# Kernel tuning notes

Hardware: AMD Instinct MI355X
Metric: run time of the kernel (lower is better)

The kernel has to match this reference:

```python
import jax, jax.numpy as jnp
import numpy as np

N, M, ND, K = 80000, 150000, 10000, 27  # active voxels, 2D painted points, downscaled voxels, 3x3x3 kernel
C3, C2, CP = 16, 64, 259                # 3D ch (stage 1), 2D conv ch, painted 2D feature ch
CM, CO = C3 + C2, 32 + 64               # mixed ch (80), downscale out ch (96)


def subm_conv(feats, nbr, W):
    """Submanifold sparse conv as gather + per-offset GEMM.
    feats: [N_in, Cin], nbr: [N_out, K] int (-1 = missing), W: [K, Cin, Cout]."""
    out = jnp.zeros((nbr.shape[0], W.shape[-1]), feats.dtype)
    for k in range(W.shape[0]):  # fixed small kernel loop (27)
        idx = nbr[:, k]
        g = jnp.where((idx >= 0)[:, None], feats[jnp.clip(idx, 0)], 0.0)
        out = out + g @ W[k]
    return out


def bn_relu(x, gamma, beta):  # folded eval-mode BN1d + ReLU
    return jax.nn.relu(x * gamma + beta)


def setup_inputs() -> dict:
    key = jax.random.key(0)
    ks = jax.random.split(key, 24)

    def w(k, shape, fan_in):
        return jax.random.normal(k, shape, jnp.float32) * (1.0 / np.sqrt(fan_in))

    inp = {
        'x3d': jax.random.normal(ks[0], (N, C3), jnp.float32),
        'f2d': jax.random.normal(ks[1], (M, CP), jnp.float32),
        'nn_idx': jax.random.randint(ks[2], (N,), -1, M, jnp.int32),     # -1 = no 2D match
        'nbr': jax.random.randint(ks[3], (N, K), -1, N, jnp.int32),      # -1 = missing neighbor
        'nbr_ds': jax.random.randint(ks[4], (ND, K), -1, N, jnp.int32),
        'W3d': w(ks[5], (K, C3, C3), K * C3),
        'g3d': jnp.ones((C3,), jnp.float32), 'b3d': jnp.zeros((C3,), jnp.float32),
        'Wg': w(ks[6], (C3, CP), C3), 'bg': jnp.zeros((CP,), jnp.float32),
        'Wc': w(ks[7], (C3, CP), C3), 'bc': jnp.zeros((CP,), jnp.float32),
        'Wp': w(ks[8], (CP, C2), CP),
        'W2d': w(ks[9], (K, C2, C2), K * C2),
        'g2d': jnp.ones((C2,), jnp.float32), 'b2d': jnp.zeros((C2,), jnp.float32),
        'Wm1': w(ks[10], (K, CM, CM), K * CM),
        'gm1': jnp.ones((CM,), jnp.float32), 'bm1': jnp.zeros((CM,), jnp.float32),
        'Wm2': w(ks[11], (K, CM, CM), K * CM),
        'gm2': jnp.ones((CM,), jnp.float32), 'bm2': jnp.zeros((CM,), jnp.float32),
        'Wa1': w(ks[12], (K, CM, CM), K * CM),
        'ga1': jnp.ones((CM,), jnp.float32), 'ba1': jnp.zeros((CM,), jnp.float32),
        'Wa2': w(ks[13], (K, CM, CM), K * CM),
        'ga2': jnp.ones((CM,), jnp.float32), 'ba2': jnp.zeros((CM,), jnp.float32),
        'Wds': w(ks[14], (K, CM, CO), K * CM),
        'gds': jnp.ones((CO,), jnp.float32), 'bds': jnp.zeros((CO,), jnp.float32),
    }
    return inp


def reference(x3d, f2d, nn_idx, nbr, nbr_ds,
              W3d, g3d, b3d, Wg, bg, Wc, bc, Wp,
              W2d, g2d, b2d,
              Wm1, gm1, bm1, Wm2, gm2, bm2,
              Wa1, ga1, ba1, Wa2, ga2, ba2,
              Wds, gds, bds):
    # irregular gather of painted 2D features to voxel sites (NN index, -1 invalid)
    f2g = jnp.where((nn_idx >= 0)[:, None], f2d[jnp.clip(nn_idx, 0)], 0.0)  # [N, 259]

    # 3D branch: SubMConv3d(C3->C3) + BN + ReLU
    y3d = bn_relu(subm_conv(x3d, nbr, W3d), g3d, b3d)                       # [N, 16]

    # per-stage gate / cross-gate (Linear + ReLU) on 3D features, applied to raw 2D feats
    gate = jax.nn.relu(y3d @ Wg + bg)                                       # [N, 259]
    cross = jax.nn.relu(y3d @ Wc + bc)                                      # [N, 259]

    # gated 2D branch: project gated painted feats to 64, SubMConv3d + BN + ReLU
    p2d = (gate * f2g) @ Wp                                                 # [N, 64]
    x2d = bn_relu(subm_conv(p2d, nbr, W2d), g2d, b2d)                       # [N, 64]
    cross2d = (cross * f2g) @ Wp                                            # [N, 64]

    # cross-modal mix + SparseBasicBlock (residual, two subm convs)
    mix = jnp.concatenate([y3d, x2d + cross2d], axis=-1)                    # [N, 80]
    h = bn_relu(subm_conv(mix, nbr, Wm1), gm1, bm1)
    h = jax.nn.relu(subm_conv(h, nbr, Wm2) * gm2 + bm2 + mix)

    # aggregation SparseBasicBlock
    a = bn_relu(subm_conv(h, nbr, Wa1), ga1, ba1)
    a = jax.nn.relu(subm_conv(a, nbr, Wa2) * ga2 + ba2 + h)

    # strided SparseConv3d downscale (gather from input sites at new out sites)
    out = bn_relu(subm_conv(a, nbr_ds, Wds), gds, bds)                      # [ND, 96]
    return out
```

## Files before the change

### kernel.cpp

```cpp
#include <hip/hip_runtime.h>

#define NPTS 80000
#define MPTS 150000
#define NDPTS 10000
#define KOFF 27
#define C3 16
#define CP 259
#define C2 64
#define CM 80
#define CO 96

typedef __attribute__((ext_vector_type(8))) short short8;
typedef __attribute__((ext_vector_type(4))) float f32x4;

__device__ inline short bf16r(float f) {
  union { float f; unsigned u; } x{f};
  unsigned r = (x.u + 0x7fffu + ((x.u >> 16) & 1u)) >> 16;
  return (short)r;
}

__global__ void wfrag_kernel(const float* __restrict__ W, short* __restrict__ WbfF,
                             int CIN, int COUT_, int KC) {
  const int NT = COUT_ / 16;
  int i = blockIdx.x * 256 + threadIdx.x;
  int total = KOFF * KC * NT * 512;
  if (i >= total) return;
  int j = i & 7, lane = (i >> 3) & 63;
  int rest = i >> 9;
  int t = rest % NT; rest /= NT;
  int q = rest % KC;
  int k = rest / KC;
  int ci = q * 32 + (lane >> 4) * 8 + j;
  int n = t * 16 + (lane & 15);
  float v = (ci < CIN) ? W[((size_t)k * CIN + ci) * COUT_ + n] : 0.f;
  WbfF[i] = bf16r(v);
}

__global__ void wpfrag_kernel(const float* __restrict__ Wp, short* __restrict__ WpF) {
  int i = blockIdx.x * 256 + threadIdx.x;
  if (i >= 9 * 4 * 64 * 8) return;
  int j = i & 7, lane = (i >> 3) & 63, t = (i >> 9) & 3, q = i >> 11;
  int k = q * 32 + (lane >> 4) * 8 + j;
  int n = t * 16 + (lane & 15);
  WpF[i] = (k < CP) ? bf16r(Wp[(size_t)k * C2 + n]) : (short)0;
}

__global__ __launch_bounds__(256) void conv3d_bnrelu_kernel(
    const float* __restrict__ x3d, const int* __restrict__ nbr,
    const float* __restrict__ W3d, const float* __restrict__ g3d,
    const float* __restrict__ b3d, float* __restrict__ y3d,
    float* __restrict__ mix, short* __restrict__ mixbf)
{
  __shared__ float wS[KOFF * C3 * C3];
  __shared__ float fS[16][C3];
  const int tid = threadIdx.x;
  const int base = blockIdx.x * 16;
  for (int e = tid; e < KOFF * C3 * C3; e += 256) wS[e] = W3d[e];
  const int r = tid >> 4, c = tid & 15;
  const int row = base + r;
  float acc = 0.f;
  for (int k = 0; k < KOFF; ++k) {
    int idx = nbr[row * KOFF + k];
    float fv = (idx >= 0) ? x3d[idx * C3 + c] : 0.f;
    __syncthreads();
    fS[r][c] = fv;
    __syncthreads();
    const float* wk = &wS[k * C3 * C3];
    #pragma unroll
    for (int ci = 0; ci < C3; ++ci)
      acc = fmaf(fS[r][ci], wk[ci * C3 + c], acc);
  }
  float v = fmaxf(fmaf(acc, g3d[c], b3d[c]), 0.f);
  y3d[row * C3 + c] = v;
  mix[row * CM + c] = v;
  mixbf[row * CM + c] = bf16r(v);
}

__global__ __launch_bounds__(256) void gate_cross_mfma_kernel(
    const float* __restrict__ y3d, const float* __restrict__ f2d,
    const int* __restrict__ nn_idx,
    const float* __restrict__ Wg, const float* __restrict__ bg,
    const float* __restrict__ Wc, const float* __restrict__ bc,
    const short* __restrict__ WpF,
    short* __restrict__ p2dbf, float* __restrict__ cross2d)
{
  constexpr int RS = 296;
  __shared__ short g1S[32 * RS];
  __shared__ short g2S[32 * RS];
  __shared__ float yS[32][C3];
  const int tid = threadIdx.x;
  const int lane = tid & 63;
  const int w = tid >> 6;
  const int lm = lane & 15;
  const int quad = lane >> 4;
  const int base = blockIdx.x * 32;

  for (int e = tid; e < 32 * 32; e += 256) {
    int r = e >> 5, cc = 256 + (e & 31);
    if (cc >= CP) {
      g1S[r * RS + cc] = 0;
      g2S[r * RS + cc] = 0;
    }
  }

  int ix[32];
  #pragma unroll
  for (int r = 0; r < 32; ++r) ix[r] = nn_idx[base + r];

  const int c = tid;
  float f[32];
  #pragma unroll
  for (int r = 0; r < 32; ++r)
    f[r] = (ix[r] >= 0) ? f2d[(size_t)ix[r] * CP + c] : 0.f;

  float ftail = 0.f;
  int tr = 0, tcc = 0;
  if (tid < 96) {
    tr = tid / 3; tcc = tid - tr * 3;
    if (ix[tr] >= 0) ftail = f2d[(size_t)ix[tr] * CP + 256 + tcc];
  }

  for (int e = tid; e < 32 * C3; e += 256)
    ((float*)yS)[e] = y3d[(size_t)base * C3 + e];

  float wg[16], wc[16];
  #pragma unroll
  for (int ci = 0; ci < 16; ++ci) {
    wg[ci] = Wg[ci * CP + c];
    wc[ci] = Wc[ci * CP + c];
  }
  const float bgv = bg[c], bcv = bc[c];

  __syncthreads();

  #pragma unroll
  for (int r = 0; r < 32; ++r) {
    float a1 = bgv, a2 = bcv;
    #pragma unroll
    for (int ci = 0; ci < 16; ++ci) {
      float yv = yS[r][ci];
      a1 = fmaf(yv, wg[ci], a1);
      a2 = fmaf(yv, wc[ci], a2);
    }
    g1S[r * RS + c] = bf16r(fmaxf(a1, 0.f) * f[r]);
    g2S[r * RS + c] = bf16r(fmaxf(a2, 0.f) * f[r]);
  }

  if (tid < 96) {
    const int c2 = 256 + tcc;
    float a1 = bg[c2], a2 = bc[c2];
    #pragma unroll
    for (int ci = 0; ci < 16; ++ci) {
      float yv = yS[tr][ci];
      a1 = fmaf(yv, Wg[ci * CP + c2], a1);
      a2 = fmaf(yv, Wc[ci * CP + c2], a2);
    }
    g1S[tr * RS + c2] = bf16r(fmaxf(a1, 0.f) * ftail);
    g2S[tr * RS + c2] = bf16r(fmaxf(a2, 0.f) * ftail);
  }
  __syncthreads();

  const int gsel = w & 1;
  const int mt = w >> 1;
  const short* gS = gsel ? g2S : g1S;
  f32x4 acc[4];
  #pragma unroll
  for (int t = 0; t < 4; ++t) {
    f32x4 z = {0.f, 0.f, 0.f, 0.f};
    acc[t] = z;
  }
  #pragma unroll
  for (int q = 0; q < 9; ++q) {
    short8 af = *(const short8*)&gS[(mt * 16 + lm) * RS + q * 32 + quad * 8];
    #pragma unroll
    for (int t = 0; t < 4; ++t) {
      short8 bf = *(const short8*)&WpF[(((q * 4 + t) * 64) + lane) * 8];
      acc[t] = __builtin_amdgcn_mfma_f32_16x16x32_bf16(af, bf, acc[t], 0, 0, 0);
    }
  }
  #pragma unroll
  for (int t = 0; t < 4; ++t) {
    const int cc = t * 16 + lm;
    #pragma unroll
    for (int rg = 0; rg < 4; ++rg) {
      const int row = base + mt * 16 + quad * 4 + rg;
      float v = acc[t][rg];
      if (gsel == 0)
        p2dbf[(size_t)row * C2 + cc] = bf16r(v);
      else
        cross2d[(size_t)row * C2 + cc] = v;
    }
  }
}

template <int CIN, int COUT_, int MODE, int MT>
__global__ __launch_bounds__(64, 2) void conv_nolds_kernel(
    const short* __restrict__ finbf, const int* __restrict__ nbr, int nrows,
    const short* __restrict__ WbfF, const float* __restrict__ gamma,
    const float* __restrict__ beta, const float* __restrict__ resf,
    float* __restrict__ outf, short* __restrict__ outbf)
{
  constexpr int KC = (CIN + 31) / 32;
  constexpr int DCH = CIN / 8;
  constexpr int NT = COUT_ / 16;

  const int lane = threadIdx.x;
  const int lm = lane & 15;
  const int quad = lane >> 4;
  const int base = blockIdx.x * (MT * 16);

  int rrow[MT];
  bool rok[MT];
  #pragma unroll
  for (int i = 0; i < MT; ++i) {
    rrow[i] = base + i * 16 + lm;
    rok[i] = rrow[i] < nrows;
  }

  f32x4 acc[MT][NT];
  #pragma unroll
  for (int i = 0; i < MT; ++i)
    #pragma unroll
    for (int t = 0; t < NT; ++t) {
      f32x4 z = {0.f, 0.f, 0.f, 0.f};
      acc[i][t] = z;
    }

  const short8 zero8 = {0, 0, 0, 0, 0, 0, 0, 0};

  auto loadIdx = [&](int (&id)[MT], int k) {
    #pragma unroll
    for (int i = 0; i < MT; ++i)
      id[i] = (k < KOFF && rok[i]) ? nbr[(size_t)rrow[i] * KOFF + k] : -1;
  };

  auto loadA = [&](short8 (&pa)[MT][KC], const int (&id)[MT]) {
    #pragma unroll
    for (int i = 0; i < MT; ++i) {
      const int safe = (id[i] < 0) ? 0 : id[i];
      const bool ok = id[i] >= 0;
      const short* src = finbf + (size_t)safe * CIN;
      #pragma unroll
      for (int q = 0; q < KC; ++q) {
        const int ch = q * 4 + quad;
        short8 v = zero8;
        if (ch < DCH) v = *(const short8*)(src + ch * 8);
        pa[i][q] = ok ? v : zero8;
      }
    }
  };

  auto computeK = [&](const short8 (&pa)[MT][KC], int k) {
    const short* wb = WbfF + ((size_t)k * KC * NT) * 512 + lane * 8;
    #pragma unroll
    for (int q = 0; q < KC; ++q) {
      #pragma unroll
      for (int t = 0; t < NT; ++t) {
        short8 bfr = *(const short8*)(wb + (q * NT + t) * 512);
        #pragma unroll
        for (int i = 0; i < MT; ++i)
          acc[i][t] = __builtin_amdgcn_mfma_f32_16x16x32_bf16(pa[i][q], bfr,
                                                              acc[i][t], 0, 0, 0);
      }
    }
  };

  int ia[MT], ib[MT], ic[MT];
  short8 paA[MT][KC], paB[MT][KC], paC[MT][KC];

  loadIdx(ia, 0); loadIdx(ib, 1); loadIdx(ic, 2);
  loadA(paA, ia); loadIdx(ia, 3);
  loadA(paB, ib); loadIdx(ib, 4);

  for (int kk = 0; kk < KOFF; kk += 3) {
    loadA(paC, ic); loadIdx(ic, kk + 5);
    computeK(paA, kk);
    loadA(paA, ia); loadIdx(ia, kk + 6);
    computeK(paB, kk + 1);
    loadA(paB, ib); loadIdx(ib, kk + 7);
    computeK(paC, kk + 2);
  }

  #pragma unroll
  for (int i = 0; i < MT; ++i) {
    int rbase = base + i * 16 + quad * 4;
    #pragma unroll
    for (int t = 0; t < NT; ++t) {
      int cc = t * 16 + lm;
      float g = gamma[cc], b = beta[cc];
      #pragma unroll
      for (int rg = 0; rg < 4; ++rg) {
        int row = rbase + rg;
        if (row >= nrows) continue;
        float v = acc[i][t][rg];
        if (MODE == 0) {
          outf[(size_t)row * COUT_ + cc] = fmaxf(fmaf(v, g, b), 0.f);
        } else if (MODE == 1) {
          outbf[(size_t)row * COUT_ + cc] = bf16r(fmaxf(fmaf(v, g, b), 0.f));
        } else if (MODE == 2) {
          float o = fmaxf(fmaf(v, g, b), 0.f) + resf[(size_t)row * C2 + cc];
          outf[(size_t)row * CM + 16 + cc] = o;
          outbf[(size_t)row * CM + 16 + cc] = bf16r(o);
        } else if (MODE == 3) {
          float o = fmaxf(fmaf(v, g, b) + resf[(size_t)row * COUT_ + cc], 0.f);
          outf[(size_t)row * COUT_ + cc] = o;
          outbf[(size_t)row * COUT_ + cc] = bf16r(o);
        } else {
          float o = fmaxf(fmaf(v, g, b) + resf[(size_t)row * COUT_ + cc], 0.f);
          outbf[(size_t)row * COUT_ + cc] = bf16r(o);
        }
      }
    }
  }
}

extern "C" void kernel_launch(void* const* d_in, const int* in_sizes, int n_in,
                              void* d_out, int out_size, void* d_ws, size_t ws_size,
                              hipStream_t stream) {
  const float* x3d  = (const float*)d_in[0];
  const float* f2d  = (const float*)d_in[1];
  const int*   nn   = (const int*)d_in[2];
  const int*   nbr  = (const int*)d_in[3];
  const int*   nbds = (const int*)d_in[4];
  const float* W3d  = (const float*)d_in[5];
  const float* g3d  = (const float*)d_in[6];
  const float* b3d  = (const float*)d_in[7];
  const float* Wg   = (const float*)d_in[8];
  const float* bg   = (const float*)d_in[9];
  const float* Wc   = (const float*)d_in[10];
  const float* bc   = (const float*)d_in[11];
  const float* Wp   = (const float*)d_in[12];
  const float* W2d  = (const float*)d_in[13];
  const float* g2d  = (const float*)d_in[14];
  const float* b2d  = (const float*)d_in[15];
  const float* Wm1  = (const float*)d_in[16];
  const float* gm1  = (const float*)d_in[17];
  const float* bm1  = (const float*)d_in[18];
  const float* Wm2  = (const float*)d_in[19];
  const float* gm2  = (const float*)d_in[20];
  const float* bm2  = (const float*)d_in[21];
  const float* Wa1  = (const float*)d_in[22];
  const float* ga1  = (const float*)d_in[23];
  const float* ba1  = (const float*)d_in[24];
  const float* Wa2  = (const float*)d_in[25];
  const float* ga2  = (const float*)d_in[26];
  const float* ba2  = (const float*)d_in[27];
  const float* Wds  = (const float*)d_in[28];
  const float* gds  = (const float*)d_in[29];
  const float* bds  = (const float*)d_in[30];

  const size_t N = NPTS;
  float* ws = (float*)d_ws;
  float* y3d     = ws;
  short* p2dbf   = (short*)(ws + N * 16);
  float* cross2d = ws + N * 48;
  float* mix     = ws + N * 112;
  short* mixbf   = (short*)(ws + N * 192);
  short* tmp1bf  = (short*)(ws + N * 232);
  float* hbuf    = ws + N * 272;
  short* hbufbf  = (short*)(ws + N * 352);
  short* abufbf  = (short*)ws;
  short* wtail  = (short*)(ws + N * 392);
  short* WbfF2d = wtail;
  short* WbfFm1 = WbfF2d + 110592;
  short* WbfFm2 = WbfFm1 + 207360;
  short* WbfFa1 = WbfFm2 + 207360;
  short* WbfFa2 = WbfFa1 + 207360;
  short* WbfFds = WbfFa2 + 207360;
  short* WpF    = WbfFds + 248832;

  wfrag_kernel<<<(110592 + 255) / 256, 256, 0, stream>>>(W2d, WbfF2d, 64, 64, 2);
  wfrag_kernel<<<(207360 + 255) / 256, 256, 0, stream>>>(Wm1, WbfFm1, 80, 80, 3);
  wfrag_kernel<<<(207360 + 255) / 256, 256, 0, stream>>>(Wm2, WbfFm2, 80, 80, 3);
  wfrag_kernel<<<(207360 + 255) / 256, 256, 0, stream>>>(Wa1, WbfFa1, 80, 80, 3);
  wfrag_kernel<<<(207360 + 255) / 256, 256, 0, stream>>>(Wa2, WbfFa2, 80, 80, 3);
  wfrag_kernel<<<(248832 + 255) / 256, 256, 0, stream>>>(Wds, WbfFds, 80, 96, 3);
  wpfrag_kernel<<<(9 * 4 * 64 * 8 + 255) / 256, 256, 0, stream>>>(Wp, WpF);

  conv3d_bnrelu_kernel<<<NPTS / 16, 256, 0, stream>>>(x3d, nbr, W3d, g3d, b3d,
                                                      y3d, mix, mixbf);
  gate_cross_mfma_kernel<<<NPTS / 32, 256, 0, stream>>>(y3d, f2d, nn, Wg, bg,
                                                        Wc, bc, WpF, p2dbf,
                                                        cross2d);

  const int gridM2 = (NPTS + 31) / 32;
  conv_nolds_kernel<64, 64, 2, 2><<<gridM2, 64, 0, stream>>>(
      p2dbf, nbr, NPTS, WbfF2d, g2d, b2d, cross2d, mix, mixbf);
  conv_nolds_kernel<80, 80, 1, 2><<<gridM2, 64, 0, stream>>>(
      mixbf, nbr, NPTS, WbfFm1, gm1, bm1, nullptr, nullptr, tmp1bf);
  conv_nolds_kernel<80, 80, 3, 2><<<gridM2, 64, 0, stream>>>(
      tmp1bf, nbr, NPTS, WbfFm2, gm2, bm2, mix, hbuf, hbufbf);
  conv_nolds_kernel<80, 80, 1, 2><<<gridM2, 64, 0, stream>>>(
      hbufbf, nbr, NPTS, WbfFa1, ga1, ba1, nullptr, nullptr, tmp1bf);
  conv_nolds_kernel<80, 80, 4, 2><<<gridM2, 64, 0, stream>>>(
      tmp1bf, nbr, NPTS, WbfFa2, ga2, ba2, hbuf, nullptr, abufbf);

  const int gridDS = (NDPTS + 15) / 16;
  conv_nolds_kernel<80, 96, 0, 1><<<gridDS, 64, 0, stream>>>(
      abufbf, nbds, NDPTS, WbfFds, gds, bds, nullptr, (float*)d_out, nullptr);
}
```

Before: 1.015 ms.

## Slice neighbor gathers by input row range and stage neighbor indices in LDS

The sparse conv kernel now runs the full 27-offset loop S times. Each pass gathers only the neighbors whose input row falls in one quarter of the input array; the others are zero-filled, so the gathered working set per pass can fit in cache. The block's neighbor index table is staged once into shared memory. Epilogue loads and stores become nontemporal. In exchange the MFMA work and weight fragment loads repeat S times, and the original prefetch of indices ahead of the gathers is dropped.

```diff
diff --git a/kernel.cpp b/kernel.cpp
--- a/kernel.cpp
+++ b/kernel.cpp
@@ -193,9 +193,10 @@
   }
 }
 
-template <int CIN, int COUT_, int MODE, int MT>
-__global__ __launch_bounds__(64, 2) void conv_nolds_kernel(
+template <int CIN, int COUT_, int MODE, int MT, int S>
+__global__ __launch_bounds__(64, 2) void conv_slice_kernel(
     const short* __restrict__ finbf, const int* __restrict__ nbr, int nrows,
+    int inrows,
     const short* __restrict__ WbfF, const float* __restrict__ gamma,
     const float* __restrict__ beta, const float* __restrict__ resf,
     float* __restrict__ outf, short* __restrict__ outbf)
@@ -204,18 +205,21 @@
   constexpr int DCH = CIN / 8;
   constexpr int NT = COUT_ / 16;
 
+  __shared__ int nbrS[MT * 16 * KOFF];
+
   const int lane = threadIdx.x;
   const int lm = lane & 15;
   const int quad = lane >> 4;
   const int base = blockIdx.x * (MT * 16);
 
-  int rrow[MT];
-  bool rok[MT];
-  #pragma unroll
-  for (int i = 0; i < MT; ++i) {
-    rrow[i] = base + i * 16 + lm;
-    rok[i] = rrow[i] < nrows;
-  }
+  for (int e = lane; e < MT * 16 * KOFF; e += 64) {
+    int r = e / KOFF;
+    int row = base + r;
+    nbrS[e] = (row < nrows)
+        ? __builtin_nontemporal_load(&nbr[(size_t)row * KOFF + (e - r * KOFF)])
+        : -1;
+  }
+  __syncthreads();
 
   f32x4 acc[MT][NT];
   #pragma unroll
@@ -228,24 +232,24 @@
 
   const short8 zero8 = {0, 0, 0, 0, 0, 0, 0, 0};
 
-  auto loadIdx = [&](int (&id)[MT], int k) {
+  auto readIdx = [&](int k, int (&id)[MT]) {
     #pragma unroll
     for (int i = 0; i < MT; ++i)
-      id[i] = (k < KOFF && rok[i]) ? nbr[(size_t)rrow[i] * KOFF + k] : -1;
+      id[i] = (k < KOFF) ? nbrS[(i * 16 + lm) * KOFF + k] : -1;
   };
 
-  auto loadA = [&](short8 (&pa)[MT][KC], const int (&id)[MT]) {
+  auto loadA = [&](short8 (&pa)[MT][KC], const int (&id)[MT], int lo, int hi) {
     #pragma unroll
     for (int i = 0; i < MT; ++i) {
-      const int safe = (id[i] < 0) ? 0 : id[i];
-      const bool ok = id[i] >= 0;
-      const short* src = finbf + (size_t)safe * CIN;
       #pragma unroll
-      for (int q = 0; q < KC; ++q) {
-        const int ch = q * 4 + quad;
-        short8 v = zero8;
-        if (ch < DCH) v = *(const short8*)(src + ch * 8);
-        pa[i][q] = ok ? v : zero8;
+      for (int q = 0; q < KC; ++q) pa[i][q] = zero8;
+      if (id[i] >= lo && id[i] < hi) {
+        const short* src = finbf + (size_t)id[i] * CIN;
+        #pragma unroll
+        for (int q = 0; q < KC; ++q) {
+          const int ch = q * 4 + quad;
+          if (ch < DCH) pa[i][q] = *(const short8*)(src + ch * 8);
+        }
       }
     }
   };
@@ -265,20 +269,25 @@
     }
   };
 
-  int ia[MT], ib[MT], ic[MT];
-  short8 paA[MT][KC], paB[MT][KC], paC[MT][KC];
-
-  loadIdx(ia, 0); loadIdx(ib, 1); loadIdx(ic, 2);
-  loadA(paA, ia); loadIdx(ia, 3);
-  loadA(paB, ib); loadIdx(ib, 4);
-
-  for (int kk = 0; kk < KOFF; kk += 3) {
-    loadA(paC, ic); loadIdx(ic, kk + 5);
-    computeK(paA, kk);
-    loadA(paA, ia); loadIdx(ia, kk + 6);
-    computeK(paB, kk + 1);
-    loadA(paB, ib); loadIdx(ib, kk + 7);
-    computeK(paC, kk + 2);
+  const int SL = inrows / S;
+
+  for (int p = 0; p < S; ++p) {
+    const int lo = p * SL;
+    const int hi = (p == S - 1) ? inrows : (lo + SL);
+
+    int idt[MT];
+    short8 paA[MT][KC], paB[MT][KC], paC[MT][KC];
+    readIdx(0, idt); loadA(paA, idt, lo, hi);
+    readIdx(1, idt); loadA(paB, idt, lo, hi);
+
+    for (int kk = 0; kk < KOFF; kk += 3) {
+      readIdx(kk + 2, idt); loadA(paC, idt, lo, hi);
+      computeK(paA, kk);
+      readIdx(kk + 3, idt); loadA(paA, idt, lo, hi);
+      computeK(paB, kk + 1);
+      readIdx(kk + 4, idt); loadA(paB, idt, lo, hi);
+      computeK(paC, kk + 2);
+    }
   }
 
   #pragma unroll
@@ -294,20 +303,25 @@
         if (row >= nrows) continue;
         float v = acc[i][t][rg];
         if (MODE == 0) {
-          outf[(size_t)row * COUT_ + cc] = fmaxf(fmaf(v, g, b), 0.f);
+          __builtin_nontemporal_store(fmaxf(fmaf(v, g, b), 0.f),
+                                      &outf[(size_t)row * COUT_ + cc]);
         } else if (MODE == 1) {
-          outbf[(size_t)row * COUT_ + cc] = bf16r(fmaxf(fmaf(v, g, b), 0.f));
+          __builtin_nontemporal_store(bf16r(fmaxf(fmaf(v, g, b), 0.f)),
+                                      &outbf[(size_t)row * COUT_ + cc]);
         } else if (MODE == 2) {
-          float o = fmaxf(fmaf(v, g, b), 0.f) + resf[(size_t)row * C2 + cc];
-          outf[(size_t)row * CM + 16 + cc] = o;
-          outbf[(size_t)row * CM + 16 + cc] = bf16r(o);
+          float r0 = __builtin_nontemporal_load(&resf[(size_t)row * C2 + cc]);
+          float o = fmaxf(fmaf(v, g, b), 0.f) + r0;
+          __builtin_nontemporal_store(o, &outf[(size_t)row * CM + 16 + cc]);
+          __builtin_nontemporal_store(bf16r(o), &outbf[(size_t)row * CM + 16 + cc]);
         } else if (MODE == 3) {
-          float o = fmaxf(fmaf(v, g, b) + resf[(size_t)row * COUT_ + cc], 0.f);
-          outf[(size_t)row * COUT_ + cc] = o;
-          outbf[(size_t)row * COUT_ + cc] = bf16r(o);
+          float r0 = __builtin_nontemporal_load(&resf[(size_t)row * COUT_ + cc]);
+          float o = fmaxf(fmaf(v, g, b) + r0, 0.f);
+          __builtin_nontemporal_store(o, &outf[(size_t)row * COUT_ + cc]);
+          __builtin_nontemporal_store(bf16r(o), &outbf[(size_t)row * COUT_ + cc]);
         } else {
-          float o = fmaxf(fmaf(v, g, b) + resf[(size_t)row * COUT_ + cc], 0.f);
-          outbf[(size_t)row * COUT_ + cc] = bf16r(o);
+          float r0 = __builtin_nontemporal_load(&resf[(size_t)row * COUT_ + cc]);
+          float o = fmaxf(fmaf(v, g, b) + r0, 0.f);
+          __builtin_nontemporal_store(bf16r(o), &outbf[(size_t)row * COUT_ + cc]);
         }
       }
     }
@@ -384,18 +398,19 @@
                                                         cross2d);
 
   const int gridM2 = (NPTS + 31) / 32;
-  conv_nolds_kernel<64, 64, 2, 2><<<gridM2, 64, 0, stream>>>(
-      p2dbf, nbr, NPTS, WbfF2d, g2d, b2d, cross2d, mix, mixbf);
-  conv_nolds_kernel<80, 80, 1, 2><<<gridM2, 64, 0, stream>>>(
-      mixbf, nbr, NPTS, WbfFm1, gm1, bm1, nullptr, nullptr, tmp1bf);
-  conv_nolds_kernel<80, 80, 3, 2><<<gridM2, 64, 0, stream>>>(
-      tmp1bf, nbr, NPTS, WbfFm2, gm2, bm2, mix, hbuf, hbufbf);
-  conv_nolds_kernel<80, 80, 1, 2><<<gridM2, 64, 0, stream>>>(
-      hbufbf, nbr, NPTS, WbfFa1, ga1, ba1, nullptr, nullptr, tmp1bf);
-  conv_nolds_kernel<80, 80, 4, 2><<<gridM2, 64, 0, stream>>>(
-      tmp1bf, nbr, NPTS, WbfFa2, ga2, ba2, hbuf, nullptr, abufbf);
+  conv_slice_kernel<64, 64, 2, 2, 4><<<gridM2, 64, 0, stream>>>(
+      p2dbf, nbr, NPTS, NPTS, WbfF2d, g2d, b2d, cross2d, mix, mixbf);
+  conv_slice_kernel<80, 80, 1, 2, 4><<<gridM2, 64, 0, stream>>>(
+      mixbf, nbr, NPTS, NPTS, WbfFm1, gm1, bm1, nullptr, nullptr, tmp1bf);
+  conv_slice_kernel<80, 80, 3, 2, 4><<<gridM2, 64, 0, stream>>>(
+      tmp1bf, nbr, NPTS, NPTS, WbfFm2, gm2, bm2, mix, hbuf, hbufbf);
+  conv_slice_kernel<80, 80, 1, 2, 4><<<gridM2, 64, 0, stream>>>(
+      hbufbf, nbr, NPTS, NPTS, WbfFa1, ga1, ba1, nullptr, nullptr, tmp1bf);
+  conv_slice_kernel<80, 80, 4, 2, 4><<<gridM2, 64, 0, stream>>>(
+      tmp1bf, nbr, NPTS, NPTS, WbfFa2, ga2, ba2, hbuf, nullptr, abufbf);
 
   const int gridDS = (NDPTS + 15) / 16;
-  conv_nolds_kernel<80, 96, 0, 1><<<gridDS, 64, 0, stream>>>(
-      abufbf, nbds, NDPTS, WbfFds, gds, bds, nullptr, (float*)d_out, nullptr);
-}
+  conv_slice_kernel<80, 96, 0, 1, 1><<<gridDS, 64, 0, stream>>>(
+      abufbf, nbds, NDPTS, NPTS, WbfFds, gds, bds, nullptr, (float*)d_out,
+      nullptr);
+}
```

After: 1.804 ms. +77.7%, slower.
